# Kernel optimization log

Measured on AMD Instinct MI355X. Metric: run time of the kernel, lower is better.

Reference implementation:

```python
import jax, jax.numpy as jnp
import numpy as np

N_GRAPHS = 512
NODES_PER_G = 200
EDGES_PER_G = 6400
N = N_GRAPHS * NODES_PER_G        # 102400 nodes
E = N_GRAPHS * EDGES_PER_G        # 3276800 edges
HID = 128
NCLS = 10


def _linear_params(key, fan_in, fan_out):
    # torch nn.Linear default init: U(-1/sqrt(fan_in), 1/sqrt(fan_in))
    s = 1.0 / np.sqrt(fan_in)
    kw, kb = jax.random.split(key)
    W = jax.random.uniform(kw, (fan_in, fan_out), minval=-s, maxval=s, dtype=jnp.float32)
    b = jax.random.uniform(kb, (fan_out,), minval=-s, maxval=s, dtype=jnp.float32)
    return W, b


def setup_inputs() -> dict:
    key = jax.random.key(0)
    ks = jax.random.split(key, 10)
    # edges are confined within each graph (DGL batched graph structure)
    g_off = (jnp.arange(E, dtype=jnp.int32) // EDGES_PER_G) * NODES_PER_G
    src = (g_off + jax.random.randint(ks[0], (E,), 0, NODES_PER_G)).astype(jnp.int32)
    dst = (g_off + jax.random.randint(ks[1], (E,), 0, NODES_PER_G)).astype(jnp.int32)
    W1, b1 = _linear_params(ks[2], 1, HID)
    W2, b2 = _linear_params(ks[3], HID, HID)
    Wa, ba = _linear_params(ks[4], HID, 512)
    Wb, bb = _linear_params(ks[5], 512, 1024)
    Wc, bc = _linear_params(ks[6], 1024, 1024)
    Wd, bd = _linear_params(ks[7], 1024, 512)
    We, be = _linear_params(ks[8], 512, NCLS)
    return dict(src=src, dst=dst, W1=W1, b1=b1, W2=W2, b2=b2,
                Wa=Wa, ba=ba, Wb=Wb, bb=bb, Wc=Wc, bc=bc,
                Wd=Wd, bd=bd, We=We, be=be)


def reference(src, dst, W1, b1, W2, b2, Wa, ba, Wb, bb, Wc, bc, Wd, bd, We, be):
    seg = jax.ops.segment_sum
    ones = jnp.ones((E,), jnp.float32)
    in_deg = seg(ones, dst, num_segments=N)    # [N]
    out_deg = seg(ones, src, num_segments=N)   # [N]
    # DGL GraphConv norm='both': degrees clamped to min 1
    inv_out = (1.0 / jnp.sqrt(jnp.maximum(out_deg, 1.0)))[:, None]
    inv_in = (1.0 / jnp.sqrt(jnp.maximum(in_deg, 1.0)))[:, None]

    def gconv(h, W, b):
        h = (h @ W) * inv_out                    # src-side normalize (weight applied first; same math)
        h = seg(h[src], dst, num_segments=N)     # gather + scatter-add aggregation
        return h * inv_in + b                    # dst-side normalize + bias

    h = in_deg[:, None]                          # input node features = in-degrees, [N,1]
    h = jax.nn.relu(gconv(h, W1, b1))
    h = jax.nn.relu(gconv(h, W2, b2))

    gid = jnp.arange(N, dtype=jnp.int32) // NODES_PER_G
    hg = seg(h, gid, num_segments=N_GRAPHS) / float(NODES_PER_G)  # mean readout, [G,HID]

    x = jax.nn.relu(hg @ Wa + ba)
    x = jax.nn.relu(x @ Wb + bb)
    x = jax.nn.relu(x @ Wc + bc)
    x = jax.nn.relu(x @ Wd + bd)
    return jax.nn.softmax(x @ We + be, axis=-1)  # nn.Softmax over class dim
```

## Files before the change

kernel.cpp:

```cpp
#include <hip/hip_runtime.h>
#include <stdint.h>

typedef unsigned short u16;
typedef unsigned int   u32;

#define NG   512
#define NPG  200
#define EPG  6400
#define NN   (NG*NPG)
#define NE_  (NG*EPG)
#define HID  128
#define KP   224
#define AP   232
#define ZP   136
#define AZ_WORDS (208*AP)

__device__ __forceinline__ float bf2f(u16 b){ u32 u = ((u32)b) << 16; return __builtin_bit_cast(float, u); }
__device__ __forceinline__ u16 f2bf(float f){
    u32 u = __builtin_bit_cast(u32, f);
    u = (u + 0x7FFFu + ((u >> 16) & 1u)) >> 16;
    return (u16)u;
}

typedef __attribute__((ext_vector_type(8))) short bf16x8;
typedef __attribute__((ext_vector_type(4))) float f32x4;

enum : int {
  O_W1 = 0,        O_b1 = 128,      O_W2 = 256,      O_b2 = 16640,
  O_Wa = 16768,    O_ba = 82304,    O_Wb = 82816,    O_bb = 607104,
  O_Wc = 608128,   O_bc = 1656704,  O_Wd = 1657728,  O_bd = 2182016,
  O_We = 2182528,  O_be = 2187648,  O_END = 2187658
};

__global__ __launch_bounds__(128) void k_detect(const u16* __restrict__ w1bits,
                                                int* __restrict__ flag)
{
    __shared__ int cnt;
    const int tid = threadIdx.x;
    if (tid == 0) cnt = 0;
    __syncthreads();
    u16 u = w1bits[tid];
    int e = (u >> 7) & 0xFF;
    if (e >= 0x7F) atomicAdd(&cnt, 1);
    __syncthreads();
    if (tid == 0) *flag = (cnt > 4) ? 1 : 0;
}

struct Cvt { const void* src[14]; int off[15]; };

__global__ __launch_bounds__(256) void k_convert(Cvt c, float* __restrict__ dst,
                                                 const int* __restrict__ flag, int total)
{
    const int f = *flag;
    int i = blockIdx.x * 256 + threadIdx.x;
    if (i >= total) return;
    int t = 0;
    while (i >= c.off[t+1]) t++;
    int j = i - c.off[t];
    dst[i] = f ? ((const float*)c.src[t])[j] : bf2f(((const u16*)c.src[t])[j]);
}

__global__ __launch_bounds__(256) void k_w2t(const void* __restrict__ w2src,
                                             const float* __restrict__ w2canon,
                                             u16* __restrict__ W2T,
                                             const int* __restrict__ flag)
{
    int i = blockIdx.x * 256 + threadIdx.x;
    if (i >= HID*HID) return;
    int outc = i >> 7, inc = i & 127;
    int jsrc = inc*HID + outc;
    W2T[i] = (*flag) ? f2bf(w2canon[jsrc]) : ((const u16*)w2src)[jsrc];
}

__global__ __launch_bounds__(256) void k_graph_l1(
    const int* __restrict__ src, const int* __restrict__ dst,
    const float* __restrict__ W1, const float* __restrict__ b1,
    float* __restrict__ invInG, u16* __restrict__ h1sT)
{
    __shared__ u16 srcL[EPG];
    __shared__ u16 dstL[EPG];
    __shared__ int degIn[NPG];
    __shared__ int degOut[NPG];
    __shared__ float sValL[NPG], sAgg[NPG], iiL[NPG], ioL[NPG], tL[NPG];
    __shared__ float w1L[HID], b1L[HID];

    const int g = blockIdx.x, tid = threadIdx.x;

    if (tid < NPG){ degIn[tid] = 0; degOut[tid] = 0; sAgg[tid] = 0.f; }
    if (tid < HID){ w1L[tid] = W1[tid]; b1L[tid] = b1[tid]; }
    __syncthreads();

    const int ebase = g * EPG;
    #pragma unroll
    for (int i = 0; i < EPG/256; i++){
        int e = i*256 + tid;
        int s = src[ebase + e] - g*NPG;
        int d = dst[ebase + e] - g*NPG;
        srcL[e] = (u16)s; dstL[e] = (u16)d;
        atomicAdd(&degOut[s], 1);
        atomicAdd(&degIn[d], 1);
    }
    __syncthreads();

    if (tid < NPG){
        int din = degIn[tid], dout = degOut[tid];
        float ii = rsqrtf(fmaxf((float)din, 1.f));
        float io = rsqrtf(fmaxf((float)dout, 1.f));
        iiL[tid] = ii; ioL[tid] = io;
        sValL[tid] = (float)din * io;
        invInG[g*NPG + tid] = ii;
    }
    __syncthreads();

    #pragma unroll
    for (int i = 0; i < EPG/256; i++){
        int e = i*256 + tid;
        atomicAdd(&sAgg[dstL[e]], sValL[srcL[e]]);
    }
    __syncthreads();

    if (tid < NPG) tL[tid] = sAgg[tid] * iiL[tid];
    __syncthreads();

    const size_t base = (size_t)g * HID * KP;
    #pragma unroll 4
    for (int i = 0; i < HID*KP/256; i++){
        int idx = i*256 + tid;
        int c = idx / KP, v = idx - c*KP;
        u16 o = 0;
        if (v < NPG)
            o = f2bf(fmaxf(fmaf(tL[v], w1L[c], b1L[c]), 0.f) * ioL[v]);
        h1sT[base + idx] = o;
    }
}

__global__ __launch_bounds__(256, 1) void k_fused_graph(
    const int* __restrict__ src, const int* __restrict__ dst,
    const u16* __restrict__ h1sT, const u16* __restrict__ W2T,
    const float* __restrict__ invInG, const float* __restrict__ b2,
    float* __restrict__ hg)
{
    __shared__ __align__(16) u16 AZ[AZ_WORDS];
    __shared__ float invInL[NPG];
    __shared__ float b2L[HID];
    __shared__ float poolL[HID];

    const int g = blockIdx.x, tid = threadIdx.x;
    u32* az32 = (u32*)AZ;

    uint4* az4 = (uint4*)AZ;
    for (int i = tid; i < AZ_WORDS/8; i += 256) az4[i] = make_uint4(0,0,0,0);
    if (tid < HID){ b2L[tid] = b2[tid]; poolL[tid] = 0.f; }
    if (tid < NPG) invInL[tid] = invInG[g*NPG + tid];
    __syncthreads();

    const int ebase = g * EPG;
    #pragma unroll
    for (int i = 0; i < EPG/256; i++){
        int e = ebase + i*256 + tid;
        int s = src[e] - g*NPG;
        int v = dst[e] - g*NPG;
        int idx = v*AP + s;
        atomicAdd(&az32[idx >> 1], 1u << (16*(idx & 1)));
    }
    __syncthreads();

    for (int i = tid; i < AZ_WORDS/2; i += 256){
        u32 wv = az32[i];
        if (wv){
            u32 lo = wv & 0xFFFFu, hi = wv >> 16;
            az32[i] = (u32)f2bf((float)lo) | ((u32)f2bf((float)hi) << 16);
        }
    }
    __syncthreads();

    const int w = tid >> 6, lane = tid & 63;
    const int lr = lane & 15, quad = lane >> 4;

    f32x4 acc[4][8];
    const f32x4 fz = {0.f, 0.f, 0.f, 0.f};
    #pragma unroll
    for (int mi = 0; mi < 4; mi++)
        #pragma unroll
        for (int nt = 0; nt < 8; nt++) acc[mi][nt] = fz;

    {
        const u16* Bg = h1sT + (size_t)g * HID * KP;
        bf16x8 bcur[8], bnxt[8];
        #pragma unroll
        for (int nt = 0; nt < 8; nt++)
            bcur[nt] = *(const bf16x8*)&Bg[(nt*16 + lr)*KP + quad*8];
        for (int ks = 0; ks < 7; ks++){
            if (ks < 6){
                #pragma unroll
                for (int nt = 0; nt < 8; nt++)
                    bnxt[nt] = *(const bf16x8*)&Bg[(nt*16 + lr)*KP + (ks+1)*32 + quad*8];
            }
            bf16x8 af[4];
            #pragma unroll
            for (int mi = 0; mi < 4; mi++){
                int mt = w + mi*4;
                if (mt < 13)
                    af[mi] = *(const bf16x8*)&AZ[(mt*16 + lr)*AP + ks*32 + quad*8];
            }
            #pragma unroll
            for (int mi = 0; mi < 4; mi++){
                int mt = w + mi*4;
                if (mt < 13){
                    #pragma unroll
                    for (int nt = 0; nt < 8; nt++)
                        acc[mi][nt] = __builtin_amdgcn_mfma_f32_16x16x32_bf16(
                            af[mi], bcur[nt], acc[mi][nt], 0, 0, 0);
                }
            }
            #pragma unroll
            for (int nt = 0; nt < 8; nt++) bcur[nt] = bnxt[nt];
        }
    }
    __syncthreads();

    #pragma unroll
    for (int mi = 0; mi < 4; mi++){
        int mt = w + mi*4;
        if (mt < 13){
            #pragma unroll
            for (int nt = 0; nt < 8; nt++){
                #pragma unroll
                for (int r = 0; r < 4; r++){
                    int v = mt*16 + quad*4 + r;
                    AZ[v*ZP + nt*16 + lr] = f2bf(acc[mi][nt][r]);
                }
            }
        }
    }
    __syncthreads();

    #pragma unroll
    for (int mi = 0; mi < 4; mi++)
        #pragma unroll
        for (int nt = 0; nt < 8; nt++) acc[mi][nt] = fz;
    {
        bf16x8 bcur[8], bnxt[8];
        #pragma unroll
        for (int nt = 0; nt < 8; nt++)
            bcur[nt] = *(const bf16x8*)&W2T[(nt*16 + lr)*HID + quad*8];
        for (int ks = 0; ks < 4; ks++){
            if (ks < 3){
                #pragma unroll
                for (int nt = 0; nt < 8; nt++)
                    bnxt[nt] = *(const bf16x8*)&W2T[(nt*16 + lr)*HID + (ks+1)*32 + quad*8];
            }
            bf16x8 af[4];
            #pragma unroll
            for (int mi = 0; mi < 4; mi++){
                int mt = w + mi*4;
                if (mt < 13)
                    af[mi] = *(const bf16x8*)&AZ[(mt*16 + lr)*ZP + ks*32 + quad*8];
            }
            #pragma unroll
            for (int mi = 0; mi < 4; mi++){
                int mt = w + mi*4;
                if (mt < 13){
                    #pragma unroll
                    for (int nt = 0; nt < 8; nt++)
                        acc[mi][nt] = __builtin_amdgcn_mfma_f32_16x16x32_bf16(
                            af[mi], bcur[nt], acc[mi][nt], 0, 0, 0);
                }
            }
            #pragma unroll
            for (int nt = 0; nt < 8; nt++) bcur[nt] = bnxt[nt];
        }
    }

    #pragma unroll
    for (int mi = 0; mi < 4; mi++){
        int mt = w + mi*4;
        if (mt < 13){
            #pragma unroll
            for (int nt = 0; nt < 8; nt++){
                int c = nt*16 + lr;
                float s = 0.f;
                #pragma unroll
                for (int r = 0; r < 4; r++){
                    int v = mt*16 + quad*4 + r;
                    if (v < NPG)
                        s += fmaxf(fmaf(acc[mi][nt][r], invInL[v], b2L[c]), 0.f);
                }
                atomicAdd(&poolL[c], s);
            }
        }
    }
    __syncthreads();
    if (tid < HID) hg[(size_t)g*HID + tid] = poolL[tid] * (1.f / NPG);
}

__global__ __launch_bounds__(256) void k_mlp(
    const float* __restrict__ A, const float* __restrict__ W,
    float* __restrict__ P, int K, int Nc, int chunk)
{
    constexpr int BM = 32, BN = 64, BK = 32;
    constexpr int LA = BM*BK/256;
    constexpr int LW = BK*BN/256;
    __shared__ __align__(16) float As[2][BK][BM + 4];
    __shared__ __align__(16) float Ws[2][BK][BN + 4];

    const int row0 = blockIdx.x * BM, col0 = blockIdx.y * BN, s = blockIdx.z;
    const int k0 = s * chunk;
    const int T = chunk / BK;
    const int tid = threadIdx.x;
    const int tm = (tid >> 4) * 2;
    const int tn = (tid & 15) * 4;

    float ra[LA], rw[LW];

    #pragma unroll
    for (int i = 0; i < LA; i++){
        int idx = i*256 + tid; int r = idx >> 5, kk = idx & 31;
        ra[i] = A[(size_t)(row0 + r)*K + k0 + kk];
    }
    #pragma unroll
    for (int i = 0; i < LW; i++){
        int idx = i*256 + tid; int kk = idx >> 6, c = idx & 63;
        rw[i] = W[(size_t)(k0 + kk)*Nc + col0 + c];
    }
    #pragma unroll
    for (int i = 0; i < LA; i++){
        int idx = i*256 + tid; int r = idx >> 5, kk = idx & 31;
        As[0][kk][r] = ra[i];
    }
    #pragma unroll
    for (int i = 0; i < LW; i++){
        int idx = i*256 + tid; int kk = idx >> 6, c = idx & 63;
        Ws[0][kk][c] = rw[i];
    }
    __syncthreads();

    float acc[2][4];
    #pragma unroll
    for (int i = 0; i < 2; i++)
        #pragma unroll
        for (int j = 0; j < 4; j++) acc[i][j] = 0.f;

    for (int t = 0; t < T-1; t++){
        const int buf = t & 1, nxt = buf ^ 1;
        const int kb = k0 + (t+1)*BK;
        #pragma unroll
        for (int i = 0; i < LA; i++){
            int idx = i*256 + tid; int r = idx >> 5, kk = idx & 31;
            ra[i] = A[(size_t)(row0 + r)*K + kb + kk];
        }
        #pragma unroll
        for (int i = 0; i < LW; i++){
            int idx = i*256 + tid; int kk = idx >> 6, c = idx & 63;
            rw[i] = W[(size_t)(kb + kk)*Nc + col0 + c];
        }
        #pragma unroll
        for (int kk = 0; kk < BK; kk++){
            float2 av = *(const float2*)&As[buf][kk][tm];
            float4 bv = *(const float4*)&Ws[buf][kk][tn];
            acc[0][0] = fmaf(av.x, bv.x, acc[0][0]); acc[0][1] = fmaf(av.x, bv.y, acc[0][1]);
            acc[0][2] = fmaf(av.x, bv.z, acc[0][2]); acc[0][3] = fmaf(av.x, bv.w, acc[0][3]);
            acc[1][0] = fmaf(av.y, bv.x, acc[1][0]); acc[1][1] = fmaf(av.y, bv.y, acc[1][1]);
            acc[1][2] = fmaf(av.y, bv.z, acc[1][2]); acc[1][3] = fmaf(av.y, bv.w, acc[1][3]);
        }
        #pragma unroll
        for (int i = 0; i < LA; i++){
            int idx = i*256 + tid; int r = idx >> 5, kk = idx & 31;
            As[nxt][kk][r] = ra[i];
        }
        #pragma unroll
        for (int i = 0; i < LW; i++){
            int idx = i*256 + tid; int kk = idx >> 6, c = idx & 63;
            Ws[nxt][kk][c] = rw[i];
        }
        __syncthreads();
    }
    {
        const int buf = (T-1) & 1;
        #pragma unroll
        for (int kk = 0; kk < BK; kk++){
            float2 av = *(const float2*)&As[buf][kk][tm];
            float4 bv = *(const float4*)&Ws[buf][kk][tn];
            acc[0][0] = fmaf(av.x, bv.x, acc[0][0]); acc[0][1] = fmaf(av.x, bv.y, acc[0][1]);
            acc[0][2] = fmaf(av.x, bv.z, acc[0][2]); acc[0][3] = fmaf(av.x, bv.w, acc[0][3]);
            acc[1][0] = fmaf(av.y, bv.x, acc[1][0]); acc[1][1] = fmaf(av.y, bv.y, acc[1][1]);
            acc[1][2] = fmaf(av.y, bv.z, acc[1][2]); acc[1][3] = fmaf(av.y, bv.w, acc[1][3]);
        }
    }

    float* Pd = P + (size_t)s * ((size_t)512 * Nc);
    #pragma unroll
    for (int i = 0; i < 2; i++){
        int r = row0 + tm + i;
        float4 v = { acc[i][0], acc[i][1], acc[i][2], acc[i][3] };
        *(float4*)&Pd[(size_t)r * Nc + col0 + tn] = v;
    }
}

__global__ __launch_bounds__(256) void k_reduce(
    const float* __restrict__ P, const float* __restrict__ bias,
    float* __restrict__ X, int MN, int Nc, int S)
{
    int e = blockIdx.x * 256 + threadIdx.x;
    int i0 = e * 4;
    if (i0 >= MN) return;
    float4 sum = *(const float4*)&P[i0];
    for (int s = 1; s < S; s++){
        float4 t = *(const float4*)&P[(size_t)s*MN + i0];
        sum.x += t.x; sum.y += t.y; sum.z += t.z; sum.w += t.w;
    }
    int col = i0 % Nc;
    float4 b = *(const float4*)&bias[col];
    sum.x = fmaxf(sum.x + b.x, 0.f);
    sum.y = fmaxf(sum.y + b.y, 0.f);
    sum.z = fmaxf(sum.z + b.z, 0.f);
    sum.w = fmaxf(sum.w + b.w, 0.f);
    *(float4*)&X[i0] = sum;
}

__global__ __launch_bounds__(64) void k_head(
    const float* __restrict__ X, const float* __restrict__ We,
    const float* __restrict__ be, void* __restrict__ out,
    const int* __restrict__ flag)
{
    const int g = blockIdx.x, lane = threadIdx.x;
    float part[10];
    #pragma unroll
    for (int c = 0; c < 10; c++) part[c] = 0.f;
    for (int k = lane; k < 512; k += 64){
        float x = X[(size_t)g*512 + k];
        #pragma unroll
        for (int c = 0; c < 10; c++) part[c] = fmaf(x, We[k*10 + c], part[c]);
    }
    #pragma unroll
    for (int c = 0; c < 10; c++){
        float v = part[c];
        for (int off = 32; off > 0; off >>= 1) v += __shfl_down(v, off);
        part[c] = v;
    }
    if (lane == 0){
        const int f = *flag;
        #pragma unroll
        for (int c = 0; c < 10; c++) part[c] += be[c];
        float m = part[0];
        #pragma unroll
        for (int c = 1; c < 10; c++) m = fmaxf(m, part[c]);
        float e[10], s = 0.f;
        #pragma unroll
        for (int c = 0; c < 10; c++){ e[c] = __expf(part[c] - m); s += e[c]; }
        float inv = 1.f / s;
        #pragma unroll
        for (int c = 0; c < 10; c++){
            float p = e[c] * inv;
            if (f) ((float*)out)[g*10 + c] = p;
            else   ((u16*)out)[g*10 + c]  = f2bf(p);
        }
    }
}

extern "C" void kernel_launch(void* const* d_in, const int* in_sizes, int n_in,
                              void* d_out, int out_size, void* d_ws, size_t ws_size,
                              hipStream_t stream)
{
    const int* src = (const int*)d_in[0];
    const int* dst = (const int*)d_in[1];

    char* ws = (char*)d_ws;
    size_t o = 0;
    int*   flag     = (int*)  (ws + o); o += 16;
    float* wcanon   = (float*)(ws + o); o += ((size_t)O_END * 4 + 15) & ~(size_t)15;
    u16*   W2T      = (u16*)  (ws + o); o += (size_t)HID * HID * 2;
    float* invIn    = (float*)(ws + o); o += (size_t)NN * 4;
    u16*   h1sT     = (u16*)  (ws + o); o += (size_t)NG * HID * KP * 2;
    float* hg       = (float*)(ws + o); o += (size_t)NG * HID * 4;
    float* X1       = (float*)(ws + o); o += (size_t)NG * 512 * 4;
    float* X2       = (float*)(ws + o); o += (size_t)NG * 1024 * 4;
    float* X3       = (float*)(ws + o); o += (size_t)NG * 1024 * 4;
    float* X4       = (float*)(ws + o); o += (size_t)NG * 512 * 4;
    float* Pp       = (float*)h1sT;
    (void)ws_size; (void)in_sizes; (void)n_in; (void)out_size;

    k_detect<<<dim3(1), dim3(128), 0, stream>>>((const u16*)d_in[2], flag);

    Cvt cv;
    const int offs[15] = {O_W1,O_b1,O_W2,O_b2,O_Wa,O_ba,O_Wb,O_bb,O_Wc,O_bc,O_Wd,O_bd,O_We,O_be,O_END};
    for (int i = 0; i < 14; i++){ cv.src[i] = d_in[2 + i]; cv.off[i] = offs[i]; }
    cv.off[14] = offs[14];
    k_convert<<<dim3((O_END + 255)/256), dim3(256), 0, stream>>>(cv, wcanon, flag, O_END);
    k_w2t<<<dim3((HID*HID + 255)/256), dim3(256), 0, stream>>>(d_in[4], wcanon + O_W2, W2T, flag);

    const float *W1 = wcanon+O_W1, *b1 = wcanon+O_b1, *b2 = wcanon+O_b2;
    const float *Wa = wcanon+O_Wa, *ba = wcanon+O_ba, *Wb = wcanon+O_Wb, *bb = wcanon+O_bb;
    const float *Wc = wcanon+O_Wc, *bc = wcanon+O_bc, *Wd = wcanon+O_Wd, *bd = wcanon+O_bd;
    const float *We = wcanon+O_We, *be = wcanon+O_be;

    k_graph_l1<<<dim3(NG), dim3(256), 0, stream>>>(
        src, dst, W1, b1, invIn, h1sT);

    k_fused_graph<<<dim3(NG), dim3(256), 0, stream>>>(
        src, dst, h1sT, W2T, invIn, b2, hg);

    k_mlp<<<dim3(16, 8, 2),  dim3(256), 0, stream>>>(hg, Wa, Pp, 128, 512, 64);
    k_reduce<<<dim3(512*512/1024), dim3(256), 0, stream>>>(Pp, ba, X1, 512*512, 512, 2);
    k_mlp<<<dim3(16, 16, 4), dim3(256), 0, stream>>>(X1, Wb, Pp, 512, 1024, 128);
    k_reduce<<<dim3(512*1024/1024), dim3(256), 0, stream>>>(Pp, bb, X2, 512*1024, 1024, 4);
    k_mlp<<<dim3(16, 16, 4), dim3(256), 0, stream>>>(X2, Wc, Pp, 1024, 1024, 256);
    k_reduce<<<dim3(512*1024/1024), dim3(256), 0, stream>>>(Pp, bc, X3, 512*1024, 1024, 4);
    k_mlp<<<dim3(16, 8, 4),  dim3(256), 0, stream>>>(X3, Wd, Pp, 1024, 512, 256);
    k_reduce<<<dim3(512*512/1024), dim3(256), 0, stream>>>(Pp, bd, X4, 512*512, 512, 4);

    k_head<<<dim3(NG), dim3(64), 0, stream>>>(X4, We, be, d_out, flag);
}
```

Before: 299.6 us.

## Split fused graph kernel into four destination-row quarters per graph

The layer-2 graph kernel now runs four blocks per graph, each owning 50 destination nodes. k_graph_l1 buckets edges into per-quarter compact buffers, so each block reads only its own edges instead of the full src/dst arrays. The smaller LDS footprint and tile counts allow four blocks per CU, which targets occupancy and the wasted 13-of-16 tile predication. Pooled outputs are combined with global atomics into a pre-zeroed hg. This adds an extra edge-buffer write and read, and silently drops edges if a quarter exceeds 2048.

```diff
diff --git a/kernel.cpp b/kernel.cpp
--- a/kernel.cpp
+++ b/kernel.cpp
@@ -13,7 +13,8 @@
 #define KP   224
 #define AP   232
 #define ZP   136
-#define AZ_WORDS (208*AP)
+#define RQ   64
+#define QCAP 2048
 
 __device__ __forceinline__ float bf2f(u16 b){ u32 u = ((u32)b) << 16; return __builtin_bit_cast(float, u); }
 __device__ __forceinline__ u16 f2bf(float f){
@@ -63,24 +64,33 @@
 __global__ __launch_bounds__(256) void k_w2t(const void* __restrict__ w2src,
                                              const float* __restrict__ w2canon,
                                              u16* __restrict__ W2T,
+                                             float* __restrict__ hg,
                                              const int* __restrict__ flag)
 {
     int i = blockIdx.x * 256 + threadIdx.x;
-    if (i >= HID*HID) return;
-    int outc = i >> 7, inc = i & 127;
-    int jsrc = inc*HID + outc;
-    W2T[i] = (*flag) ? f2bf(w2canon[jsrc]) : ((const u16*)w2src)[jsrc];
+    if (i < HID*HID){
+        int outc = i >> 7, inc = i & 127;
+        int jsrc = inc*HID + outc;
+        W2T[i] = (*flag) ? f2bf(w2canon[jsrc]) : ((const u16*)w2src)[jsrc];
+    }
+    #pragma unroll
+    for (int k = 0; k < 4; k++){
+        int j = blockIdx.x * 1024 + k*256 + threadIdx.x;
+        if (j < NG*HID) hg[j] = 0.f;
+    }
 }
 
 __global__ __launch_bounds__(256) void k_graph_l1(
     const int* __restrict__ src, const int* __restrict__ dst,
     const float* __restrict__ W1, const float* __restrict__ b1,
-    float* __restrict__ invInG, u16* __restrict__ h1sT)
+    float* __restrict__ invInG, u16* __restrict__ h1sT,
+    u32* __restrict__ edgeBuf, int* __restrict__ cntQ)
 {
     __shared__ u16 srcL[EPG];
     __shared__ u16 dstL[EPG];
     __shared__ int degIn[NPG];
     __shared__ int degOut[NPG];
+    __shared__ int qcur[4];
     __shared__ float sValL[NPG], sAgg[NPG], iiL[NPG], ioL[NPG], tL[NPG];
     __shared__ float w1L[HID], b1L[HID];
 
@@ -88,6 +98,7 @@
 
     if (tid < NPG){ degIn[tid] = 0; degOut[tid] = 0; sAgg[tid] = 0.f; }
     if (tid < HID){ w1L[tid] = W1[tid]; b1L[tid] = b1[tid]; }
+    if (tid < 4) qcur[tid] = 0;
     __syncthreads();
 
     const int ebase = g * EPG;
@@ -115,10 +126,16 @@
     #pragma unroll
     for (int i = 0; i < EPG/256; i++){
         int e = i*256 + tid;
-        atomicAdd(&sAgg[dstL[e]], sValL[srcL[e]]);
-    }
-    __syncthreads();
-
+        int s = srcL[e], d = dstL[e];
+        atomicAdd(&sAgg[d], sValL[s]);
+        int q = (d * 41) >> 11;
+        int pos = atomicAdd(&qcur[q], 1);
+        if (pos < QCAP)
+            edgeBuf[((size_t)(g*4 + q))*QCAP + pos] = (u32)s | ((u32)(d - q*50) << 16);
+    }
+    __syncthreads();
+
+    if (tid < 4) cntQ[g*4 + tid] = (qcur[tid] < QCAP) ? qcur[tid] : QCAP;
     if (tid < NPG) tL[tid] = sAgg[tid] * iiL[tid];
     __syncthreads();
 
@@ -134,164 +151,146 @@
     }
 }
 
-__global__ __launch_bounds__(256, 1) void k_fused_graph(
-    const int* __restrict__ src, const int* __restrict__ dst,
+__global__ __launch_bounds__(256, 4) void k_fused_graph(
+    const u32* __restrict__ edgeBuf, const int* __restrict__ cntQ,
     const u16* __restrict__ h1sT, const u16* __restrict__ W2T,
     const float* __restrict__ invInG, const float* __restrict__ b2,
     float* __restrict__ hg)
 {
-    __shared__ __align__(16) u16 AZ[AZ_WORDS];
-    __shared__ float invInL[NPG];
+    __shared__ __align__(16) u16 AZ[RQ*AP];
+    __shared__ float invInL[RQ];
     __shared__ float b2L[HID];
     __shared__ float poolL[HID];
 
-    const int g = blockIdx.x, tid = threadIdx.x;
+    const int bid = blockIdx.x, tid = threadIdx.x;
+    const int g = bid >> 2, q = bid & 3;
     u32* az32 = (u32*)AZ;
-
     uint4* az4 = (uint4*)AZ;
-    for (int i = tid; i < AZ_WORDS/8; i += 256) az4[i] = make_uint4(0,0,0,0);
+
+    #pragma unroll
+    for (int i = 0; i < 8; i++){
+        int idx = i*256 + tid;
+        if (idx < RQ*AP/8) az4[idx] = make_uint4(0,0,0,0);
+    }
     if (tid < HID){ b2L[tid] = b2[tid]; poolL[tid] = 0.f; }
-    if (tid < NPG) invInL[tid] = invInG[g*NPG + tid];
-    __syncthreads();
-
-    const int ebase = g * EPG;
-    #pragma unroll
-    for (int i = 0; i < EPG/256; i++){
-        int e = ebase + i*256 + tid;
-        int s = src[e] - g*NPG;
-        int v = dst[e] - g*NPG;
-        int idx = v*AP + s;
+    if (tid < RQ) invInL[tid] = (tid < 50) ? invInG[g*NPG + q*50 + tid] : 0.f;
+    __syncthreads();
+
+    const int cnt = cntQ[bid];
+    const u32* eb = edgeBuf + (size_t)bid * QCAP;
+    for (int i = tid; i < cnt; i += 256){
+        u32 e = eb[i];
+        int s = e & 0xFFFF, dl = e >> 16;
+        int idx = dl*AP + s;
         atomicAdd(&az32[idx >> 1], 1u << (16*(idx & 1)));
     }
     __syncthreads();
 
-    for (int i = tid; i < AZ_WORDS/2; i += 256){
+    for (int i = tid; i < RQ*AP/2; i += 256){
         u32 wv = az32[i];
-        if (wv){
-            u32 lo = wv & 0xFFFFu, hi = wv >> 16;
-            az32[i] = (u32)f2bf((float)lo) | ((u32)f2bf((float)hi) << 16);
-        }
+        if (wv)
+            az32[i] = (u32)f2bf((float)(wv & 0xFFFFu)) | ((u32)f2bf((float)(wv >> 16)) << 16);
     }
     __syncthreads();
 
     const int w = tid >> 6, lane = tid & 63;
+    const int wm = w >> 1, wn = w & 1;
     const int lr = lane & 15, quad = lane >> 4;
 
-    f32x4 acc[4][8];
+    f32x4 acc[2][4];
     const f32x4 fz = {0.f, 0.f, 0.f, 0.f};
     #pragma unroll
-    for (int mi = 0; mi < 4; mi++)
-        #pragma unroll
-        for (int nt = 0; nt < 8; nt++) acc[mi][nt] = fz;
+    for (int mi = 0; mi < 2; mi++)
+        #pragma unroll
+        for (int nt = 0; nt < 4; nt++) acc[mi][nt] = fz;
 
     {
-        const u16* Bg = h1sT + (size_t)g * HID * KP;
-        bf16x8 bcur[8], bnxt[8];
-        #pragma unroll
-        for (int nt = 0; nt < 8; nt++)
+        const u16* Bg = h1sT + (size_t)g * HID * KP + (size_t)(wn*64) * KP;
+        bf16x8 bcur[4], bnxt[4];
+        #pragma unroll
+        for (int nt = 0; nt < 4; nt++)
             bcur[nt] = *(const bf16x8*)&Bg[(nt*16 + lr)*KP + quad*8];
         for (int ks = 0; ks < 7; ks++){
             if (ks < 6){
                 #pragma unroll
-                for (int nt = 0; nt < 8; nt++)
+                for (int nt = 0; nt < 4; nt++)
                     bnxt[nt] = *(const bf16x8*)&Bg[(nt*16 + lr)*KP + (ks+1)*32 + quad*8];
             }
-            bf16x8 af[4];
-            #pragma unroll
-            for (int mi = 0; mi < 4; mi++){
-                int mt = w + mi*4;
-                if (mt < 13)
-                    af[mi] = *(const bf16x8*)&AZ[(mt*16 + lr)*AP + ks*32 + quad*8];
+            bf16x8 af[2];
+            #pragma unroll
+            for (int mi = 0; mi < 2; mi++)
+                af[mi] = *(const bf16x8*)&AZ[((wm*2 + mi)*16 + lr)*AP + ks*32 + quad*8];
+            #pragma unroll
+            for (int mi = 0; mi < 2; mi++)
+                #pragma unroll
+                for (int nt = 0; nt < 4; nt++)
+                    acc[mi][nt] = __builtin_amdgcn_mfma_f32_16x16x32_bf16(
+                        af[mi], bcur[nt], acc[mi][nt], 0, 0, 0);
+            #pragma unroll
+            for (int nt = 0; nt < 4; nt++) bcur[nt] = bnxt[nt];
+        }
+    }
+    __syncthreads();
+
+    #pragma unroll
+    for (int mi = 0; mi < 2; mi++)
+        #pragma unroll
+        for (int nt = 0; nt < 4; nt++)
+            #pragma unroll
+            for (int r = 0; r < 4; r++){
+                int v = (wm*2 + mi)*16 + quad*4 + r;
+                int c = wn*64 + nt*16 + lr;
+                AZ[v*ZP + c] = f2bf(acc[mi][nt][r]);
             }
-            #pragma unroll
-            for (int mi = 0; mi < 4; mi++){
-                int mt = w + mi*4;
-                if (mt < 13){
-                    #pragma unroll
-                    for (int nt = 0; nt < 8; nt++)
-                        acc[mi][nt] = __builtin_amdgcn_mfma_f32_16x16x32_bf16(
-                            af[mi], bcur[nt], acc[mi][nt], 0, 0, 0);
-                }
-            }
-            #pragma unroll
-            for (int nt = 0; nt < 8; nt++) bcur[nt] = bnxt[nt];
-        }
-    }
-    __syncthreads();
-
-    #pragma unroll
-    for (int mi = 0; mi < 4; mi++){
-        int mt = w + mi*4;
-        if (mt < 13){
-            #pragma unroll
-            for (int nt = 0; nt < 8; nt++){
-                #pragma unroll
-                for (int r = 0; r < 4; r++){
-                    int v = mt*16 + quad*4 + r;
-                    AZ[v*ZP + nt*16 + lr] = f2bf(acc[mi][nt][r]);
-                }
-            }
-        }
-    }
-    __syncthreads();
-
-    #pragma unroll
-    for (int mi = 0; mi < 4; mi++)
-        #pragma unroll
-        for (int nt = 0; nt < 8; nt++) acc[mi][nt] = fz;
+    __syncthreads();
+
+    #pragma unroll
+    for (int mi = 0; mi < 2; mi++)
+        #pragma unroll
+        for (int nt = 0; nt < 4; nt++) acc[mi][nt] = fz;
     {
-        bf16x8 bcur[8], bnxt[8];
-        #pragma unroll
-        for (int nt = 0; nt < 8; nt++)
-            bcur[nt] = *(const bf16x8*)&W2T[(nt*16 + lr)*HID + quad*8];
+        const u16* Wg = W2T + (size_t)(wn*64) * HID;
+        bf16x8 bcur[4], bnxt[4];
+        #pragma unroll
+        for (int nt = 0; nt < 4; nt++)
+            bcur[nt] = *(const bf16x8*)&Wg[(nt*16 + lr)*HID + quad*8];
         for (int ks = 0; ks < 4; ks++){
             if (ks < 3){
                 #pragma unroll
-                for (int nt = 0; nt < 8; nt++)
-                    bnxt[nt] = *(const bf16x8*)&W2T[(nt*16 + lr)*HID + (ks+1)*32 + quad*8];
+                for (int nt = 0; nt < 4; nt++)
+                    bnxt[nt] = *(const bf16x8*)&Wg[(nt*16 + lr)*HID + (ks+1)*32 + quad*8];
             }
-            bf16x8 af[4];
-            #pragma unroll
-            for (int mi = 0; mi < 4; mi++){
-                int mt = w + mi*4;
-                if (mt < 13)
-                    af[mi] = *(const bf16x8*)&AZ[(mt*16 + lr)*ZP + ks*32 + quad*8];
+            bf16x8 af[2];
+            #pragma unroll
+            for (int mi = 0; mi < 2; mi++)
+                af[mi] = *(const bf16x8*)&AZ[((wm*2 + mi)*16 + lr)*ZP + ks*32 + quad*8];
+            #pragma unroll
+            for (int mi = 0; mi < 2; mi++)
+                #pragma unroll
+                for (int nt = 0; nt < 4; nt++)
+                    acc[mi][nt] = __builtin_amdgcn_mfma_f32_16x16x32_bf16(
+                        af[mi], bcur[nt], acc[mi][nt], 0, 0, 0);
+            #pragma unroll
+            for (int nt = 0; nt < 4; nt++) bcur[nt] = bnxt[nt];
+        }
+    }
+
+    #pragma unroll
+    for (int mi = 0; mi < 2; mi++)
+        #pragma unroll
+        for (int nt = 0; nt < 4; nt++){
+            int c = wn*64 + nt*16 + lr;
+            float s = 0.f;
+            #pragma unroll
+            for (int r = 0; r < 4; r++){
+                int v = (wm*2 + mi)*16 + quad*4 + r;
+                if (v < 50)
+                    s += fmaxf(fmaf(acc[mi][nt][r], invInL[v], b2L[c]), 0.f);
             }
-            #pragma unroll
-            for (int mi = 0; mi < 4; mi++){
-                int mt = w + mi*4;
-                if (mt < 13){
-                    #pragma unroll
-                    for (int nt = 0; nt < 8; nt++)
-                        acc[mi][nt] = __builtin_amdgcn_mfma_f32_16x16x32_bf16(
-                            af[mi], bcur[nt], acc[mi][nt], 0, 0, 0);
-                }
-            }
-            #pragma unroll
-            for (int nt = 0; nt < 8; nt++) bcur[nt] = bnxt[nt];
-        }
-    }
-
-    #pragma unroll
-    for (int mi = 0; mi < 4; mi++){
-        int mt = w + mi*4;
-        if (mt < 13){
-            #pragma unroll
-            for (int nt = 0; nt < 8; nt++){
-                int c = nt*16 + lr;
-                float s = 0.f;
-                #pragma unroll
-                for (int r = 0; r < 4; r++){
-                    int v = mt*16 + quad*4 + r;
-                    if (v < NPG)
-                        s += fmaxf(fmaf(acc[mi][nt][r], invInL[v], b2L[c]), 0.f);
-                }
-                atomicAdd(&poolL[c], s);
-            }
-        }
-    }
-    __syncthreads();
-    if (tid < HID) hg[(size_t)g*HID + tid] = poolL[tid] * (1.f / NPG);
+            atomicAdd(&poolL[c], s);
+        }
+    __syncthreads();
+    if (tid < HID) atomicAdd(&hg[(size_t)g*HID + tid], poolL[tid] * (1.f / NPG));
 }
 
 __global__ __launch_bounds__(256) void k_mlp(
@@ -471,6 +470,8 @@
     float* wcanon   = (float*)(ws + o); o += ((size_t)O_END * 4 + 15) & ~(size_t)15;
     u16*   W2T      = (u16*)  (ws + o); o += (size_t)HID * HID * 2;
     float* invIn    = (float*)(ws + o); o += (size_t)NN * 4;
+    u32*   edgeBuf  = (u32*)  (ws + o); o += (size_t)NG * 4 * QCAP * 4;
+    int*   cntQ     = (int*)  (ws + o); o += (size_t)NG * 4 * 4;
     u16*   h1sT     = (u16*)  (ws + o); o += (size_t)NG * HID * KP * 2;
     float* hg       = (float*)(ws + o); o += (size_t)NG * HID * 4;
     float* X1       = (float*)(ws + o); o += (size_t)NG * 512 * 4;
@@ -487,7 +488,7 @@
     for (int i = 0; i < 14; i++){ cv.src[i] = d_in[2 + i]; cv.off[i] = offs[i]; }
     cv.off[14] = offs[14];
     k_convert<<<dim3((O_END + 255)/256), dim3(256), 0, stream>>>(cv, wcanon, flag, O_END);
-    k_w2t<<<dim3((HID*HID + 255)/256), dim3(256), 0, stream>>>(d_in[4], wcanon + O_W2, W2T, flag);
+    k_w2t<<<dim3(64), dim3(256), 0, stream>>>(d_in[4], wcanon + O_W2, W2T, hg, flag);
 
     const float *W1 = wcanon+O_W1, *b1 = wcanon+O_b1, *b2 = wcanon+O_b2;
     const float *Wa = wcanon+O_Wa, *ba = wcanon+O_ba, *Wb = wcanon+O_Wb, *bb = wcanon+O_bb;
@@ -495,10 +496,10 @@
     const float *We = wcanon+O_We, *be = wcanon+O_be;
 
     k_graph_l1<<<dim3(NG), dim3(256), 0, stream>>>(
-        src, dst, W1, b1, invIn, h1sT);
-
-    k_fused_graph<<<dim3(NG), dim3(256), 0, stream>>>(
-        src, dst, h1sT, W2T, invIn, b2, hg);
+        src, dst, W1, b1, invIn, h1sT, edgeBuf, cntQ);
+
+    k_fused_graph<<<dim3(NG*4), dim3(256), 0, stream>>>(
+        edgeBuf, cntQ, h1sT, W2T, invIn, b2, hg);
 
     k_mlp<<<dim3(16, 8, 2),  dim3(256), 0, stream>>>(hg, Wa, Pp, 128, 512, 64);
     k_reduce<<<dim3(512*512/1024), dim3(256), 0, stream>>>(Pp, ba, X1, 512*512, 512, 2);
```

New measurement: 293.2 us. 1.02x faster.
